# Performance work log

Measured on AMD Instinct MI355X. Metric: run time of the kernel, lower is better.

## Reference

```python
import jax, jax.numpy as jnp
import numpy as np

B, C, H, W = 16, 1024, 32, 32
M = 32

def setup_inputs() -> dict:
    key = jax.random.key(0)
    k1, k2 = jax.random.split(key)
    features = jax.random.normal(k1, (B, C, H, W), dtype=jnp.float32)
    raw_attentions = jax.random.normal(k2, (B, M, H, W), dtype=jnp.float32)
    return {"features": features, "raw_attentions": raw_attentions}

def reference(features, raw_attentions):
    # non_lin='sigmoid'
    attentions = jax.nn.sigmoid(raw_attentions)  # [B, M, H, W]
    # GAP pooling of features * attentions[:, i] for each map i, fused as one
    # contraction: feature_matrix[b, m, c] = mean_{h,w} features[b,c,h,w] * att[b,m,h,w]
    hw = features.shape[2] * features.shape[3]
    feature_matrix = jnp.einsum('bchw,bmhw->bmc', features, attentions) / hw  # [B, M, C]
    return feature_matrix, attentions
```

## Files before the change

### kernel.cpp

```cpp
#include <hip/hip_runtime.h>
#include <cstdint>
#include <cstddef>


#define BB 16
#define CC 1024
#define MM 32
#define HW 1024

#define TCR 32
#define TKF 128
#define NSTF (HW / TKF)

typedef __attribute__((ext_vector_type(4))) float f32x4;
typedef __attribute__((ext_vector_type(8))) float f32x8;
typedef __attribute__((ext_vector_type(8))) short s16x8;

__device__ inline short bf16rne(float x)
{
    uint32_t u = __builtin_bit_cast(uint32_t, x);
    u = (u + 0x7FFFu + ((u >> 16) & 1u)) >> 16;
    return (short)u;
}

__device__ inline s16x8 cvt8(f32x4 lo, f32x4 hi)
{
    s16x8 r;
#pragma unroll
    for (int j = 0; j < 4; ++j) {
        r[j]     = bf16rne(lo[j]);
        r[4 + j] = bf16rne(hi[j]);
    }
    return r;
}

__device__ inline void gld_lds16(const void* g, void* l)
{
    __builtin_amdgcn_global_load_lds(
        (const __attribute__((address_space(1))) void*)g,
        (__attribute__((address_space(3))) void*)l, 16, 0, 0);
}

__global__ __launch_bounds__(256) void sigmoid_kernel(
    const float* __restrict__ raw, float* __restrict__ out1,
    unsigned short* __restrict__ ws)
{
    int g = blockIdx.x * 256 + threadIdx.x;
    f32x8 v = reinterpret_cast<const f32x8*>(raw)[g];
    f32x8 s;
    s16x8 h;
#pragma unroll
    for (int j = 0; j < 8; ++j) {
        s[j] = 1.0f / (1.0f + __expf(-v[j]));
        h[j] = bf16rne(s[j]);
    }
    reinterpret_cast<f32x8*>(out1)[g] = s;
    reinterpret_cast<s16x8*>(ws)[g] = h;
}

__global__ __launch_bounds__(256) void bap_mfma(
    const float* __restrict__ feat,
    const unsigned short* __restrict__ ws,
    float* __restrict__ out0)
{
    __shared__ float fsh[2][TCR][TKF];

    const int t  = threadIdx.x;
    const int w  = t >> 6;
    const int l  = t & 63;
    const int b  = blockIdx.x & 15;
    const int ct = blockIdx.x >> 4;
    const int cbase = ct * TCR;

    const int lrow  = l >> 5;
    const int lslot = l & 31;

    const float* fbase = feat + (size_t)(b * CC + cbase) * HW;

    auto stage = [&](int s, int nb) {
        const int k0 = s * TKF;
#pragma unroll
        for (int i = 0; i < 4; ++i) {
            int r0  = w * 8 + i * 2;
            int row = r0 + lrow;
            int sg  = lslot ^ (row & 15);
            gld_lds16(fbase + (size_t)row * HW + k0 + sg * 4,
                      &fsh[nb][r0][0]);
        }
    };

    const int r  = l & 15;
    const int q  = l >> 4;
    const int mt = w >> 1;
    const int c2 = w & 1;
    const int arow = mt * 16 + r;
    const int brow = c2 * 16 + r;
    const s16x8* ap = reinterpret_cast<const s16x8*>(
        ws + (size_t)(b * MM + arow) * HW);

    s16x8 af[2][4];
    auto load_af = [&](int s, int pb) {
#pragma unroll
        for (int ch = 0; ch < 4; ++ch)
            af[pb][ch] = ap[s * 16 + ch * 4 + q];
    };

    f32x4 acc = {0.f, 0.f, 0.f, 0.f};

    auto compute = [&](int s, int nb, int pb) {
#pragma unroll
        for (int ch = 0; ch < 4; ++ch) {
            const int S0 = ch * 8 + 2 * q;
            f32x4 blo = *reinterpret_cast<const f32x4*>(
                &fsh[nb][brow][(S0 ^ r) * 4]);
            f32x4 bhi = *reinterpret_cast<const f32x4*>(
                &fsh[nb][brow][((S0 + 1) ^ r) * 4]);
            acc = __builtin_amdgcn_mfma_f32_16x16x32_bf16(
                      af[pb][ch], cvt8(blo, bhi), acc, 0, 0, 0);
        }
    };

    load_af(0, 0);
    stage(0, 0);
    __syncthreads();
#pragma unroll
    for (int s = 0; s < NSTF; ++s) {
        if (s + 1 < NSTF) {
            load_af(s + 1, (s + 1) & 1);
            stage(s + 1, (s + 1) & 1);
        }
        compute(s, s & 1, s & 1);
        __syncthreads();
    }

    const float sc = 1.0f / (float)HW;
    float* p = out0 + (size_t)(b * MM) * CC + cbase + c2 * 16;
#pragma unroll
    for (int reg = 0; reg < 4; ++reg)
        p[(size_t)(mt * 16 + 4 * q + reg) * CC + r] = acc[reg] * sc;
}

extern "C" void kernel_launch(void* const* d_in, const int* in_sizes, int n_in,
                              void* d_out, int out_size, void* d_ws, size_t ws_size,
                              hipStream_t stream)
{
    const float* feat = (const float*)d_in[0];
    const float* raw  = (const float*)d_in[1];
    float* out0 = (float*)d_out;
    float* out1 = out0 + (size_t)BB * MM * HW;
    unsigned short* att_bf = (unsigned short*)d_ws;

    sigmoid_kernel<<<256, 256, 0, stream>>>(raw, out1, att_bf);
    bap_mfma<<<512, 256, 0, stream>>>(feat, att_bf, out0);
}
```

Baseline: 22.65 us.

## Deepen load pipeline to four stages with explicit vmcnt waits

The double buffer becomes a four-slot ring for the feature tiles in LDS and the attention fragments in registers, so three stages of global loads stay in flight. The full __syncthreads is replaced by a manual s_waitcnt vmcnt count plus s_barrier, and the attention loads use inline asm so the counter arithmetic matches. This aims to hide global memory latency in the memory-bound GEMV-like contraction. In exchange LDS use doubles to 64KB, which lowers occupancy, and register pressure rises. The hand-counted vmcnt values are fragile if the compiler emits its loads differently.

```diff
diff --git a/kernel.cpp b/kernel.cpp
--- a/kernel.cpp
+++ b/kernel.cpp
@@ -11,6 +11,7 @@
 #define TCR 32
 #define TKF 128
 #define NSTF (HW / TKF)
+#define ND 4
 
 typedef __attribute__((ext_vector_type(4))) float f32x4;
 typedef __attribute__((ext_vector_type(8))) float f32x8;
@@ -63,7 +64,7 @@
     const unsigned short* __restrict__ ws,
     float* __restrict__ out0)
 {
-    __shared__ float fsh[2][TCR][TKF];
+    __shared__ float fsh[ND][TCR][TKF];
 
     const int t  = threadIdx.x;
     const int w  = t >> 6;
@@ -77,7 +78,8 @@
 
     const float* fbase = feat + (size_t)(b * CC + cbase) * HW;
 
-    auto stage = [&](int s, int nb) {
+    auto stage = [&](int s) {
+        const int nb = s & (ND - 1);
         const int k0 = s * TKF;
 #pragma unroll
         for (int i = 0; i < 4; ++i) {
@@ -98,16 +100,21 @@
     const s16x8* ap = reinterpret_cast<const s16x8*>(
         ws + (size_t)(b * MM + arow) * HW);
 
-    s16x8 af[2][4];
-    auto load_af = [&](int s, int pb) {
+    s16x8 af[ND][4];
+    auto load_af = [&](int s) {
+        const int pb = s & (ND - 1);
 #pragma unroll
-        for (int ch = 0; ch < 4; ++ch)
-            af[pb][ch] = ap[s * 16 + ch * 4 + q];
+        for (int ch = 0; ch < 4; ++ch) {
+            const s16x8* a = ap + s * 16 + ch * 4 + q;
+            asm volatile("global_load_dwordx4 %0, %1, off"
+                         : "=&v"(af[pb][ch]) : "v"(a) : "memory");
+        }
     };
 
     f32x4 acc = {0.f, 0.f, 0.f, 0.f};
 
-    auto compute = [&](int s, int nb, int pb) {
+    auto compute = [&](int s) {
+        const int nb = s & (ND - 1);
 #pragma unroll
         for (int ch = 0; ch < 4; ++ch) {
             const int S0 = ch * 8 + 2 * q;
@@ -116,21 +123,24 @@
             f32x4 bhi = *reinterpret_cast<const f32x4*>(
                 &fsh[nb][brow][((S0 + 1) ^ r) * 4]);
             acc = __builtin_amdgcn_mfma_f32_16x16x32_bf16(
-                      af[pb][ch], cvt8(blo, bhi), acc, 0, 0, 0);
+                      af[nb][ch], cvt8(blo, bhi), acc, 0, 0, 0);
         }
     };
 
-    load_af(0, 0);
-    stage(0, 0);
-    __syncthreads();
+    load_af(0); stage(0);
+    load_af(1); stage(1);
+    load_af(2); stage(2);
+
 #pragma unroll
     for (int s = 0; s < NSTF; ++s) {
-        if (s + 1 < NSTF) {
-            load_af(s + 1, (s + 1) & 1);
-            stage(s + 1, (s + 1) & 1);
-        }
-        compute(s, s & 1, s & 1);
-        __syncthreads();
+        const int rem = NSTF - 1 - s;
+        if (rem >= 2)      asm volatile("s_waitcnt vmcnt(16)" ::: "memory");
+        else if (rem == 1) asm volatile("s_waitcnt vmcnt(8)"  ::: "memory");
+        else               asm volatile("s_waitcnt vmcnt(0)"  ::: "memory");
+        __builtin_amdgcn_sched_barrier(0);
+        __builtin_amdgcn_s_barrier();
+        if (s + 3 < NSTF) { load_af(s + 3); stage(s + 3); }
+        compute(s);
     }
 
     const float sc = 1.0f / (float)HW;
```

Result: no change. 22.66 us (+0.1%).
